# Kernel optimization log

Hardware: AMD Instinct MI355X
Metric: run time of the kernel (lower is better)

Reference implementation:

```python
import jax, jax.numpy as jnp
import numpy as np

IN1, IN2, OUT = 256, 64, 64

def setup_inputs() -> dict:
    key = jax.random.key(0)
    k1, k2, k3, k4 = jax.random.split(key, 4)
    x1 = jax.random.normal(k1, (4, 4096, IN1), dtype=jnp.float32)
    x2 = jax.random.normal(k2, (4, 4096, IN2), dtype=jnp.float32)
    # nn.Linear(in_1, in_2*out): weight (in_2*out, in_1), bias (in_2*out,)
    W = jax.random.normal(k3, (IN2 * OUT, IN1), dtype=jnp.float32) / np.sqrt(IN1)
    bvec = jax.random.normal(k4, (IN2 * OUT,), dtype=jnp.float32) * 0.01
    return {"x1": x1, "x2": x2, "W": W, "bvec": bvec}

def reference(x1, x2, W, bvec):
    b, n, _ = x1.shape
    # per-token generated weight: (b, n, in_2, out)
    w = (jnp.einsum('bni,oi->bno', x1, W) + bvec).reshape(b, n, IN2, OUT)
    # batched vector-matrix product per token
    y = jnp.einsum('bnj,bnjo->bno', x2, w)
    return y
```

## Files before the change

kernel.cpp:

```cpp
#include <hip/hip_runtime.h>


#define NFRAG 17
#define FRAG_SHORTS 512
#define OH_SHORTS (NFRAG * FRAG_SHORTS)
#define J_SHORTS  (2 * OH_SHORTS)

typedef __bf16 bf16x8 __attribute__((ext_vector_type(8)));
typedef float  f32x16 __attribute__((ext_vector_type(16)));

static __device__ __forceinline__ unsigned short f2bf(float f) {
  union { float f; unsigned u; } v; v.f = f;
  unsigned r = v.u + 0x7FFFu + ((v.u >> 16) & 1u);
  return (unsigned short)(r >> 16);
}

__global__ void prep_w(const float* __restrict__ W, const float* __restrict__ bv,
                       unsigned short* __restrict__ Wf) {
  int idx = blockIdx.x * 256 + threadIdx.x;
  int r  = idx >> 4;
  int ks = idx & 15;
  int j   = r >> 6;
  int o   = r & 63;
  int oh  = o >> 5;
  int l31 = o & 31;
  size_t fb = ((size_t)(j * 2 + oh) * NFRAG + ks) * FRAG_SHORTS;

  const float4* row = (const float4*)(W + (size_t)r * 256 + ks * 16);
  float4 v0 = row[0], v1 = row[1], v2 = row[2], v3 = row[3];
  ushort4 lo0, lo1, hi0, hi1;
  lo0.x = f2bf(v0.x); lo0.y = f2bf(v0.y); lo0.z = f2bf(v0.z); lo0.w = f2bf(v0.w);
  lo1.x = f2bf(v1.x); lo1.y = f2bf(v1.y); lo1.z = f2bf(v1.z); lo1.w = f2bf(v1.w);
  hi0.x = f2bf(v2.x); hi0.y = f2bf(v2.y); hi0.z = f2bf(v2.z); hi0.w = f2bf(v2.w);
  hi1.x = f2bf(v3.x); hi1.y = f2bf(v3.y); hi1.z = f2bf(v3.z); hi1.w = f2bf(v3.w);
  *(ushort4*)&Wf[fb + l31 * 8 + 0] = lo0;
  *(ushort4*)&Wf[fb + l31 * 8 + 4] = lo1;
  *(ushort4*)&Wf[fb + 256 + l31 * 8 + 0] = hi0;
  *(ushort4*)&Wf[fb + 256 + l31 * 8 + 4] = hi1;

  if (ks == 0) {
    size_t bb = ((size_t)(j * 2 + oh) * NFRAG + 16) * FRAG_SHORTS;
    ushort4 b0; b0.x = f2bf(bv[r]); b0.y = 0; b0.z = 0; b0.w = 0;
    ushort4 zz; zz.x = 0; zz.y = 0; zz.z = 0; zz.w = 0;
    *(ushort4*)&Wf[bb + l31 * 8 + 0] = b0;
    *(ushort4*)&Wf[bb + l31 * 8 + 4] = zz;
    *(ushort4*)&Wf[bb + 256 + l31 * 8 + 0] = zz;
    *(ushort4*)&Wf[bb + 256 + l31 * 8 + 4] = zz;
  }
}

__global__ __launch_bounds__(256, 1)
void meta_main(const float* __restrict__ x1, const float* __restrict__ x2,
               const unsigned short* __restrict__ Wf, float* __restrict__ out) {
  __shared__ unsigned short sX1[64 * 280];
  __shared__ float sX2[64 * 64];

  const int tid  = threadIdx.x;
  const int lane = tid & 63;
  const int wv   = tid >> 6;
  const int th   = wv & 1;
  const int oh   = wv >> 1;
  const int l31  = lane & 31;
  const int lg   = lane >> 5;
  const long tile0 = (long)blockIdx.x * 64;

  {
    const float4* src = (const float4*)(x1 + tile0 * 256);
    #pragma unroll
    for (int it = 0; it < 16; ++it) {
      int fi4 = it * 256 + tid;
      float4 v = src[fi4];
      int token = fi4 >> 6;
      int col   = (fi4 & 63) * 4;
      ushort4 b;
      b.x = f2bf(v.x); b.y = f2bf(v.y); b.z = f2bf(v.z); b.w = f2bf(v.w);
      *(ushort4*)&sX1[token * 280 + col] = b;
    }
    if (tid < 64) {
      ushort4 one; one.x = 0x3F80u; one.y = 0; one.z = 0; one.w = 0;
      ushort4 zz;  zz.x = 0; zz.y = 0; zz.z = 0; zz.w = 0;
      *(ushort4*)&sX1[tid * 280 + 256] = one;
      *(ushort4*)&sX1[tid * 280 + 260] = zz;
      *(ushort4*)&sX1[tid * 280 + 264] = zz;
      *(ushort4*)&sX1[tid * 280 + 268] = zz;
    }
    const float4* s2 = (const float4*)(x2 + tile0 * 64);
    #pragma unroll
    for (int it = 0; it < 4; ++it) {
      int fi4 = it * 256 + tid;
      float4 v = s2[fi4];
      int token = fi4 >> 4;
      int j0    = (fi4 & 15) * 4;
      sX2[(j0 + 0) * 64 + token] = v.x;
      sX2[(j0 + 1) * 64 + token] = v.y;
      sX2[(j0 + 2) * 64 + token] = v.z;
      sX2[(j0 + 3) * 64 + token] = v.w;
    }
  }
  __syncthreads();

  bf16x8 bfrag[NFRAG];
  {
    const unsigned short* base = &sX1[(32 * th + l31) * 280 + lg * 8];
    #pragma unroll
    for (int ks = 0; ks < NFRAG; ++ks)
      bfrag[ks] = *(const bf16x8*)(base + ks * 16);
  }

  f32x16 yacc;
  #pragma unroll
  for (int r = 0; r < 16; ++r) yacc[r] = 0.0f;

  const int tt = 32 * th + l31;
  const unsigned short* wbase = Wf + (size_t)oh * OH_SHORTS + lane * 8;

  bf16x8 wa[NFRAG], wb[NFRAG];
  #pragma unroll
  for (int ks = 0; ks < NFRAG; ++ks)
    wa[ks] = *(const bf16x8*)(wbase + ks * FRAG_SHORTS);

  for (int j = 0; j < 64; j += 2) {
    if (j + 1 < 64) {
      const unsigned short* p = wbase + (size_t)(j + 1) * J_SHORTS;
      #pragma unroll
      for (int ks = 0; ks < NFRAG; ++ks)
        wb[ks] = *(const bf16x8*)(p + ks * FRAG_SHORTS);
    }
    {
      float x2s = sX2[j * 64 + tt];
      f32x16 wlo, whi;
      #pragma unroll
      for (int r = 0; r < 16; ++r) { wlo[r] = 0.0f; whi[r] = 0.0f; }
      #pragma unroll
      for (int ks = 0; ks < 8; ++ks)
        wlo = __builtin_amdgcn_mfma_f32_32x32x16_bf16(wa[ks], bfrag[ks], wlo, 0, 0, 0);
      #pragma unroll
      for (int ks = 8; ks < NFRAG; ++ks)
        whi = __builtin_amdgcn_mfma_f32_32x32x16_bf16(wa[ks], bfrag[ks], whi, 0, 0, 0);
      #pragma unroll
      for (int r = 0; r < 16; ++r)
        yacc[r] += x2s * (wlo[r] + whi[r]);
    }
    if (j + 2 < 64) {
      const unsigned short* p = wbase + (size_t)(j + 2) * J_SHORTS;
      #pragma unroll
      for (int ks = 0; ks < NFRAG; ++ks)
        wa[ks] = *(const bf16x8*)(p + ks * FRAG_SHORTS);
    }
    {
      float x2s = sX2[(j + 1) * 64 + tt];
      f32x16 wlo, whi;
      #pragma unroll
      for (int r = 0; r < 16; ++r) { wlo[r] = 0.0f; whi[r] = 0.0f; }
      #pragma unroll
      for (int ks = 0; ks < 8; ++ks)
        wlo = __builtin_amdgcn_mfma_f32_32x32x16_bf16(wb[ks], bfrag[ks], wlo, 0, 0, 0);
      #pragma unroll
      for (int ks = 8; ks < NFRAG; ++ks)
        whi = __builtin_amdgcn_mfma_f32_32x32x16_bf16(wb[ks], bfrag[ks], whi, 0, 0, 0);
      #pragma unroll
      for (int r = 0; r < 16; ++r)
        yacc[r] += x2s * (wlo[r] + whi[r]);
    }
  }

  float* yout = out + (tile0 + tt) * 64 + oh * 32;
  #pragma unroll
  for (int r = 0; r < 16; ++r) {
    int ol = (r & 3) + 8 * (r >> 2) + 4 * lg;
    yout[ol] = yacc[r];
  }
}

extern "C" void kernel_launch(void* const* d_in, const int* in_sizes, int n_in,
                              void* d_out, int out_size, void* d_ws, size_t ws_size,
                              hipStream_t stream) {
  const float* x1 = (const float*)d_in[0];
  const float* x2 = (const float*)d_in[1];
  const float* W  = (const float*)d_in[2];
  const float* bv = (const float*)d_in[3];
  float* y = (float*)d_out;
  unsigned short* Wf = (unsigned short*)d_ws;

  prep_w<<<256, 256, 0, stream>>>(W, bv, Wf);
  meta_main<<<256, 256, 0, stream>>>(x1, x2, Wf, y);
}
```

Measured before the change: 114.4 us.

## Stage weight fragments through LDS with async loads and split bias out

Removes the bias fragment from the MFMA K-loop and computes the bias term x2·b in a separate prep_bias kernel that writes out first; the main kernel then accumulates into out. The main kernel now splits the j range across wave pairs and the output halves across blocks (512 blocks, two per CU). It streams weight fragments into a double-buffered LDS ring via global_load_lds instead of holding them in registers, and reduces the two j halves through shared memory. This cuts MFMA work by one fragment in seventeen and lowers register pressure to allow higher occupancy. In exchange it adds an extra kernel launch, a per-iteration barrier, and LDS traffic for the weights.

New measurement: 119.5 us. 1.04x slower.

```diff
diff --git a/kernel.cpp b/kernel.cpp
--- a/kernel.cpp
+++ b/kernel.cpp
@@ -1,10 +1,9 @@
 #include <hip/hip_runtime.h>
 
 
-#define NFRAG 17
+#define FRAGS 16
 #define FRAG_SHORTS 512
-#define OH_SHORTS (NFRAG * FRAG_SHORTS)
-#define J_SHORTS  (2 * OH_SHORTS)
+#define JF_SHORTS (FRAGS * FRAG_SHORTS)
 
 typedef __bf16 bf16x8 __attribute__((ext_vector_type(8)));
 typedef float  f32x16 __attribute__((ext_vector_type(16)));
@@ -15,7 +14,14 @@
   return (unsigned short)(r >> 16);
 }
 
-__global__ void prep_w(const float* __restrict__ W, const float* __restrict__ bv,
+static __device__ __forceinline__ void gload_lds16(const unsigned short* g,
+                                                   unsigned short* l) {
+  __builtin_amdgcn_global_load_lds(
+      (const __attribute__((address_space(1))) void*)g,
+      (__attribute__((address_space(3))) void*)l, 16, 0, 0);
+}
+
+__global__ void prep_w(const float* __restrict__ W,
                        unsigned short* __restrict__ Wf) {
   int idx = blockIdx.x * 256 + threadIdx.x;
   int r  = idx >> 4;
@@ -24,7 +30,7 @@
   int o   = r & 63;
   int oh  = o >> 5;
   int l31 = o & 31;
-  size_t fb = ((size_t)(j * 2 + oh) * NFRAG + ks) * FRAG_SHORTS;
+  size_t fb = ((size_t)(j * 2 + oh) * FRAGS + ks) * FRAG_SHORTS;
 
   const float4* row = (const float4*)(W + (size_t)r * 256 + ks * 16);
   float4 v0 = row[0], v1 = row[1], v2 = row[2], v3 = row[3];
@@ -37,34 +43,47 @@
   *(ushort4*)&Wf[fb + l31 * 8 + 4] = lo1;
   *(ushort4*)&Wf[fb + 256 + l31 * 8 + 0] = hi0;
   *(ushort4*)&Wf[fb + 256 + l31 * 8 + 4] = hi1;
-
-  if (ks == 0) {
-    size_t bb = ((size_t)(j * 2 + oh) * NFRAG + 16) * FRAG_SHORTS;
-    ushort4 b0; b0.x = f2bf(bv[r]); b0.y = 0; b0.z = 0; b0.w = 0;
-    ushort4 zz; zz.x = 0; zz.y = 0; zz.z = 0; zz.w = 0;
-    *(ushort4*)&Wf[bb + l31 * 8 + 0] = b0;
-    *(ushort4*)&Wf[bb + l31 * 8 + 4] = zz;
-    *(ushort4*)&Wf[bb + 256 + l31 * 8 + 0] = zz;
-    *(ushort4*)&Wf[bb + 256 + l31 * 8 + 4] = zz;
-  }
-}
-
-__global__ __launch_bounds__(256, 1)
+}
+
+__global__ void prep_bias(const float* __restrict__ x2,
+                          const float* __restrict__ bv,
+                          float* __restrict__ out) {
+  __shared__ float sbv[4096];
+  __shared__ float sx2[256];
+  int tid = threadIdx.x;
+  #pragma unroll
+  for (int i = 0; i < 16; ++i) sbv[i * 256 + tid] = bv[i * 256 + tid];
+  long t0 = (long)blockIdx.x * 4;
+  sx2[tid] = x2[t0 * 64 + tid];
+  __syncthreads();
+  int o = tid & 63, tl = tid >> 6;
+  float acc = 0.f;
+  #pragma unroll
+  for (int j = 0; j < 64; ++j) acc += sx2[tl * 64 + j] * sbv[j * 64 + o];
+  out[(t0 + tl) * 64 + o] = acc;
+}
+
+__global__ __launch_bounds__(256, 2)
 void meta_main(const float* __restrict__ x1, const float* __restrict__ x2,
                const unsigned short* __restrict__ Wf, float* __restrict__ out) {
-  __shared__ unsigned short sX1[64 * 280];
+  __shared__ unsigned short sWf[4 * JF_SHORTS];
   __shared__ float sX2[64 * 64];
 
   const int tid  = threadIdx.x;
   const int lane = tid & 63;
   const int wv   = tid >> 6;
   const int th   = wv & 1;
-  const int oh   = wv >> 1;
+  const int jh   = wv >> 1;
   const int l31  = lane & 31;
   const int lg   = lane >> 5;
-  const long tile0 = (long)blockIdx.x * 64;
+
+  const int bid  = blockIdx.x;
+  const int oh   = (bid >> 3) & 1;
+  const int tile = (bid & 7) + ((bid >> 4) << 3);
+  const long tile0 = (long)tile * 64;
 
   {
+    unsigned short* sX1 = sWf;
     const float4* src = (const float4*)(x1 + tile0 * 256);
     #pragma unroll
     for (int it = 0; it < 16; ++it) {
@@ -74,15 +93,7 @@
       int col   = (fi4 & 63) * 4;
       ushort4 b;
       b.x = f2bf(v.x); b.y = f2bf(v.y); b.z = f2bf(v.z); b.w = f2bf(v.w);
-      *(ushort4*)&sX1[token * 280 + col] = b;
-    }
-    if (tid < 64) {
-      ushort4 one; one.x = 0x3F80u; one.y = 0; one.z = 0; one.w = 0;
-      ushort4 zz;  zz.x = 0; zz.y = 0; zz.z = 0; zz.w = 0;
-      *(ushort4*)&sX1[tid * 280 + 256] = one;
-      *(ushort4*)&sX1[tid * 280 + 260] = zz;
-      *(ushort4*)&sX1[tid * 280 + 264] = zz;
-      *(ushort4*)&sX1[tid * 280 + 268] = zz;
+      *(ushort4*)&sX1[token * 264 + col] = b;
     }
     const float4* s2 = (const float4*)(x2 + tile0 * 64);
     #pragma unroll
@@ -99,76 +110,77 @@
   }
   __syncthreads();
 
-  bf16x8 bfrag[NFRAG];
+  bf16x8 bfrag[FRAGS];
   {
-    const unsigned short* base = &sX1[(32 * th + l31) * 280 + lg * 8];
-    #pragma unroll
-    for (int ks = 0; ks < NFRAG; ++ks)
+    const unsigned short* base = &sWf[(32 * th + l31) * 264 + lg * 8];
+    #pragma unroll
+    for (int ks = 0; ks < FRAGS; ++ks)
       bfrag[ks] = *(const bf16x8*)(base + ks * 16);
   }
+  __syncthreads();
+
+  const int jbase = jh * 32;
+  unsigned short* ring = &sWf[jh * 2 * JF_SHORTS];
+  const unsigned short* wlane =
+      Wf + ((size_t)(jbase * 2 + oh)) * JF_SHORTS + lane * 8;
+
+  if (th == 0) {
+    #pragma unroll
+    for (int ks = 0; ks < FRAGS; ++ks)
+      gload_lds16(wlane + ks * FRAG_SHORTS, &ring[ks * FRAG_SHORTS]);
+  }
+  __syncthreads();
 
   f32x16 yacc;
   #pragma unroll
   for (int r = 0; r < 16; ++r) yacc[r] = 0.0f;
 
   const int tt = 32 * th + l31;
-  const unsigned short* wbase = Wf + (size_t)oh * OH_SHORTS + lane * 8;
-
-  bf16x8 wa[NFRAG], wb[NFRAG];
-  #pragma unroll
-  for (int ks = 0; ks < NFRAG; ++ks)
-    wa[ks] = *(const bf16x8*)(wbase + ks * FRAG_SHORTS);
-
-  for (int j = 0; j < 64; j += 2) {
-    if (j + 1 < 64) {
-      const unsigned short* p = wbase + (size_t)(j + 1) * J_SHORTS;
+
+  #pragma unroll 2
+  for (int jl = 0; jl < 32; ++jl) {
+    const int buf = jl & 1;
+    if (th == 0 && jl + 1 < 32) {
+      const unsigned short* p = wlane + (size_t)(jl + 1) * 2 * JF_SHORTS;
+      unsigned short* d = &ring[(buf ^ 1) * JF_SHORTS];
       #pragma unroll
-      for (int ks = 0; ks < NFRAG; ++ks)
-        wb[ks] = *(const bf16x8*)(p + ks * FRAG_SHORTS);
-    }
-    {
-      float x2s = sX2[j * 64 + tt];
-      f32x16 wlo, whi;
-      #pragma unroll
-      for (int r = 0; r < 16; ++r) { wlo[r] = 0.0f; whi[r] = 0.0f; }
-      #pragma unroll
-      for (int ks = 0; ks < 8; ++ks)
-        wlo = __builtin_amdgcn_mfma_f32_32x32x16_bf16(wa[ks], bfrag[ks], wlo, 0, 0, 0);
-      #pragma unroll
-      for (int ks = 8; ks < NFRAG; ++ks)
-        whi = __builtin_amdgcn_mfma_f32_32x32x16_bf16(wa[ks], bfrag[ks], whi, 0, 0, 0);
-      #pragma unroll
-      for (int r = 0; r < 16; ++r)
-        yacc[r] += x2s * (wlo[r] + whi[r]);
-    }
-    if (j + 2 < 64) {
-      const unsigned short* p = wbase + (size_t)(j + 2) * J_SHORTS;
-      #pragma unroll
-      for (int ks = 0; ks < NFRAG; ++ks)
-        wa[ks] = *(const bf16x8*)(p + ks * FRAG_SHORTS);
-    }
-    {
-      float x2s = sX2[(j + 1) * 64 + tt];
-      f32x16 wlo, whi;
-      #pragma unroll
-      for (int r = 0; r < 16; ++r) { wlo[r] = 0.0f; whi[r] = 0.0f; }
-      #pragma unroll
-      for (int ks = 0; ks < 8; ++ks)
-        wlo = __builtin_amdgcn_mfma_f32_32x32x16_bf16(wb[ks], bfrag[ks], wlo, 0, 0, 0);
-      #pragma unroll
-      for (int ks = 8; ks < NFRAG; ++ks)
-        whi = __builtin_amdgcn_mfma_f32_32x32x16_bf16(wb[ks], bfrag[ks], whi, 0, 0, 0);
-      #pragma unroll
-      for (int r = 0; r < 16; ++r)
-        yacc[r] += x2s * (wlo[r] + whi[r]);
-    }
-  }
-
-  float* yout = out + (tile0 + tt) * 64 + oh * 32;
-  #pragma unroll
-  for (int r = 0; r < 16; ++r) {
-    int ol = (r & 3) + 8 * (r >> 2) + 4 * lg;
-    yout[ol] = yacc[r];
+      for (int ks = 0; ks < FRAGS; ++ks)
+        gload_lds16(p + ks * FRAG_SHORTS, d + ks * FRAG_SHORTS);
+    }
+    const unsigned short* rb = &ring[buf * JF_SHORTS] + lane * 8;
+    f32x16 wlo, whi;
+    #pragma unroll
+    for (int r = 0; r < 16; ++r) { wlo[r] = 0.0f; whi[r] = 0.0f; }
+    #pragma unroll
+    for (int ks = 0; ks < 8; ++ks) {
+      bf16x8 wk = *(const bf16x8*)(rb + ks * FRAG_SHORTS);
+      wlo = __builtin_amdgcn_mfma_f32_32x32x16_bf16(wk, bfrag[ks], wlo, 0, 0, 0);
+    }
+    #pragma unroll
+    for (int ks = 8; ks < 16; ++ks) {
+      bf16x8 wk = *(const bf16x8*)(rb + ks * FRAG_SHORTS);
+      whi = __builtin_amdgcn_mfma_f32_32x32x16_bf16(wk, bfrag[ks], whi, 0, 0, 0);
+    }
+    float x2s = sX2[(jbase + jl) * 64 + tt];
+    #pragma unroll
+    for (int r = 0; r < 16; ++r) yacc[r] += x2s * (wlo[r] + whi[r]);
+    __syncthreads();
+  }
+
+  float* red = (float*)sWf;
+  if (jh == 1) {
+    #pragma unroll
+    for (int r = 0; r < 16; ++r) red[(th * 64 + lane) * 17 + r] = yacc[r];
+  }
+  __syncthreads();
+  if (jh == 0) {
+    const float* rd = &red[(th * 64 + lane) * 17];
+    float* yout = out + (tile0 + tt) * 64 + oh * 32;
+    #pragma unroll
+    for (int r = 0; r < 16; ++r) {
+      int ol = (r & 3) + 8 * (r >> 2) + 4 * lg;
+      yout[ol] += yacc[r] + rd[r];
+    }
   }
 }
 
@@ -182,6 +194,7 @@
   float* y = (float*)d_out;
   unsigned short* Wf = (unsigned short*)d_ws;
 
-  prep_w<<<256, 256, 0, stream>>>(W, bv, Wf);
-  meta_main<<<256, 256, 0, stream>>>(x1, x2, Wf, y);
-}
+  prep_w<<<256, 256, 0, stream>>>(W, Wf);
+  prep_bias<<<4096, 256, 0, stream>>>(x2, bv, y);
+  meta_main<<<512, 256, 0, stream>>>(x1, x2, Wf, y);
+}
```
